# Optimization experiments

Hardware: AMD Instinct MI355X
Metric: run time of the kernel (lower is better)

## Reference

```python
import jax, jax.numpy as jnp
import numpy as np

D_MODEL = 2048
N_HEADS = 16
N_KV_HEADS = 4
D_K = D_MODEL // N_HEADS  # 128
N_REP = N_HEADS // N_KV_HEADS  # 4
EPS = 1e-8
ROPE_BASE = 10000.0


def setup_inputs() -> dict:
    key = jax.random.key(0)
    ks = jax.random.split(key, 6)
    B, S = 2, 2048
    s_in = 1.0 / np.sqrt(D_MODEL)
    return {
        "x": jax.random.normal(ks[0], (B, S, D_MODEL), jnp.float32),
        "Wq": jax.random.normal(ks[1], (D_MODEL, D_MODEL), jnp.float32) * s_in,
        "bq": jnp.zeros((D_MODEL,), jnp.float32),
        "Wk": jax.random.normal(ks[2], (N_KV_HEADS * D_K, D_MODEL), jnp.float32) * s_in,
        "bk": jnp.zeros((N_KV_HEADS * D_K,), jnp.float32),
        "Wv": jax.random.normal(ks[3], (N_KV_HEADS * D_K, D_MODEL), jnp.float32) * s_in,
        "bv": jnp.zeros((N_KV_HEADS * D_K,), jnp.float32),
        "Wo": jax.random.normal(ks[4], (D_MODEL, D_MODEL), jnp.float32) * s_in,
        "bo": jnp.zeros((D_MODEL,), jnp.float32),
        "q_norm_w": jnp.ones((D_K,), jnp.float32),
        "k_norm_w": jnp.ones((D_K,), jnp.float32),
    }


def _rmsnorm(x, w):
    rms = jnp.sqrt(jnp.mean(x * x, axis=-1, keepdims=True) + EPS)
    return x / rms * w


def _rope(x, cos, sin):
    # x: [B, S, H, d_k]; interleaved pair rotation (pairs along last dim)
    B, S, H, d = x.shape
    xr = x.reshape(B, S, H, d // 2, 2)
    x1, x2 = xr[..., 0], xr[..., 1]
    c = cos[:, None, :]  # [S, 1, d/2] -> broadcasts over [B, S, H, d/2]
    s = sin[:, None, :]
    o1 = x1 * c - x2 * s
    o2 = x1 * s + x2 * c
    return jnp.stack([o1, o2], axis=-1).reshape(B, S, H, d)


def reference(x, Wq, bq, Wk, bk, Wv, bv, Wo, bo, q_norm_w, k_norm_w):
    B, S, D = x.shape
    scale = 1.0 / np.sqrt(D_K)

    q = (x @ Wq.T + bq).reshape(B, S, N_HEADS, D_K)
    k = (x @ Wk.T + bk).reshape(B, S, N_KV_HEADS, D_K)
    v = (x @ Wv.T + bv).reshape(B, S, N_KV_HEADS, D_K)

    q = _rmsnorm(q, q_norm_w)
    k = _rmsnorm(k, k_norm_w)

    # RoPE tables (cos/sin of t * inv_freq), shape [S, d_k/2]
    inv_freq = 1.0 / (ROPE_BASE ** (jnp.arange(0, D_K, 2, dtype=jnp.float32) / D_K))
    freqs = jnp.arange(S, dtype=jnp.float32)[:, None] * inv_freq[None, :]
    cos, sin = jnp.cos(freqs), jnp.sin(freqs)
    q = _rope(q, cos, sin)
    k = _rope(k, cos, sin)

    # [B, H, S, d]
    q = q.transpose(0, 2, 1, 3)
    k = k.transpose(0, 2, 1, 3)
    v = v.transpose(0, 2, 1, 3)

    # GQA: group q heads by kv head instead of repeating k/v
    qg = q.reshape(B, N_KV_HEADS, N_REP, S, D_K)
    scores = jnp.einsum("bkrqd,bkld->bkrql", qg, k) * scale
    causal = jnp.tril(jnp.ones((S, S), dtype=bool))  # [S, S]
    scores = jnp.where(causal, scores, jnp.float32(-1e9))
    attn = jax.nn.softmax(scores, axis=-1)
    out = jnp.einsum("bkrql,bkld->bkrqd", attn, v)  # [B, Hk, rep, S, d]
    out = out.reshape(B, N_HEADS, S, D_K).transpose(0, 2, 1, 3).reshape(B, S, D)
    return out @ Wo.T + bo
```

## Files before the change

### kernel.cpp

```cpp
#include <hip/hip_runtime.h>
#include <hip/hip_bf16.h>
#include <stdint.h>

#define DM 2048
#define SQ 2048
#define NB 2
#define NH 16
#define NKV 4
#define DK 128
#define NQKV 3072

typedef unsigned short u16;
typedef unsigned int u32;
typedef __attribute__((ext_vector_type(8))) __bf16 bf16x8;
typedef __attribute__((ext_vector_type(4))) float f32x4;
typedef __attribute__((ext_vector_type(8))) u16 u16x8;
typedef __attribute__((ext_vector_type(2))) u32 u32x2;

__device__ __forceinline__ u16 f2bf(float f) {
  u32 x = __builtin_bit_cast(u32, f);
  x += 0x7fffu + ((x >> 16) & 1u);
  return (u16)(x >> 16);
}

__device__ __forceinline__ float bf2f(u16 h) {
  u32 x = ((u32)h) << 16;
  return __builtin_bit_cast(float, x);
}

__device__ __forceinline__ f32x4 mfma16(bf16x8 a, bf16x8 b, f32x4 c) {
  return __builtin_amdgcn_mfma_f32_16x16x32_bf16(a, b, c, 0, 0, 0);
}

#define GLDS16(g, l)                                                          \
  __builtin_amdgcn_global_load_lds(                                           \
      (const __attribute__((address_space(1))) void*)(g),                     \
      (__attribute__((address_space(3))) void*)(l), 16, 0, 0)

#define N_CAST 2359296
#define N_ROPE (SQ * 64)
__global__ void setup_all(const float* __restrict__ x, const float* __restrict__ Wq,
                          const float* __restrict__ Wk, const float* __restrict__ Wv,
                          const float* __restrict__ Wo, const float* __restrict__ bq,
                          const float* __restrict__ bk, const float* __restrict__ bv,
                          u16* __restrict__ xb, u16* __restrict__ Wqkvb, u16* __restrict__ Wob,
                          float* __restrict__ ct, float* __restrict__ st_,
                          float* __restrict__ fb) {
  int i = blockIdx.x * blockDim.x + threadIdx.x;
  if (i < N_CAST) {
    const float* src;
    u16* dst;
    int j;
    if (i < 1048576) { src = x; dst = xb; j = i; }
    else if (i < 1572864) { src = Wq; dst = Wqkvb; j = i - 1048576; }
    else if (i < 1703936) { src = Wk; dst = Wqkvb + (size_t)DM * DM; j = i - 1572864; }
    else if (i < 1835008) { src = Wv; dst = Wqkvb + (size_t)(DM + NKV * DK) * DM; j = i - 1703936; }
    else { src = Wo; dst = Wob; j = i - 1835008; }
    const float4* s4 = (const float4*)src;
    float4 a = s4[2 * j], b = s4[2 * j + 1];
    u16x8 v;
    v[0] = f2bf(a.x); v[1] = f2bf(a.y); v[2] = f2bf(a.z); v[3] = f2bf(a.w);
    v[4] = f2bf(b.x); v[5] = f2bf(b.y); v[6] = f2bf(b.z); v[7] = f2bf(b.w);
    *(u16x8*)(dst + 8 * (size_t)j) = v;
  } else if (i < N_CAST + N_ROPE) {
    int j = i - N_CAST;
    int s = j >> 6, d = j & 63;
    float theta = (float)s * __expf((float)d * (-9.2103403720f / 64.0f));
    float sn, cs;
    sincosf(theta, &sn, &cs);
    ct[j] = cs;
    st_[j] = sn;
  } else if (i < N_CAST + N_ROPE + NQKV) {
    int j = i - N_CAST - N_ROPE;
    float v;
    if (j < DM) v = bq[j];
    else if (j < DM + NKV * DK) v = bk[j - DM];
    else v = bv[j - DM - NKV * DK];
    fb[j] = v;
  }
}

__global__ __launch_bounds__(256) void gemm_bt(
    const u16* __restrict__ A, const u16* __restrict__ W,
    const float* __restrict__ bias, void* __restrict__ Cv,
    int M, int N, int K, int obf16) {
  __shared__ u16 As[128 * 64];
  __shared__ u16 Bs[128 * 64];
  const int tid = threadIdx.x;
  const int w = tid >> 6, l = tid & 63;
  const int hi = l >> 4, lo = l & 15;
  const int MB = M >> 7;
  const int bm = blockIdx.x % MB, bn = blockIdx.x / MB;
  const int wr = w >> 1, wc = w & 1;
  const int lr8 = l >> 3, lc = l & 7;
  f32x4 acc[4][4] = {};
  for (int kt = 0; kt < K; kt += 64) {
#pragma unroll
    for (int i = 0; i < 4; ++i) {
      int row = w * 32 + i * 8 + lr8;
      int gc = lc ^ (row & 7);
      GLDS16(A + (size_t)(bm * 128 + row) * K + kt + gc * 8, &As[(w * 32 + i * 8) * 64]);
    }
#pragma unroll
    for (int i = 0; i < 4; ++i) {
      int row = w * 32 + i * 8 + lr8;
      int gc = lc ^ (row & 7);
      GLDS16(W + (size_t)(bn * 128 + row) * K + kt + gc * 8, &Bs[(w * 32 + i * 8) * 64]);
    }
    __syncthreads();
#pragma unroll
    for (int kk = 0; kk < 2; ++kk) {
      bf16x8 af[4], bf[4];
#pragma unroll
      for (int mi = 0; mi < 4; ++mi) {
        int row = wr * 64 + mi * 16 + lo;
        af[mi] = *(const bf16x8*)&As[row * 64 + (((kk * 4 + hi) ^ (row & 7)) * 8)];
      }
#pragma unroll
      for (int ni = 0; ni < 4; ++ni) {
        int row = wc * 64 + ni * 16 + lo;
        bf[ni] = *(const bf16x8*)&Bs[row * 64 + (((kk * 4 + hi) ^ (row & 7)) * 8)];
      }
#pragma unroll
      for (int mi = 0; mi < 4; ++mi)
#pragma unroll
        for (int ni = 0; ni < 4; ++ni)
          acc[mi][ni] = mfma16(af[mi], bf[ni], acc[mi][ni]);
    }
    __syncthreads();
  }
#pragma unroll
  for (int mi = 0; mi < 4; ++mi) {
#pragma unroll
    for (int ni = 0; ni < 4; ++ni) {
      int col = bn * 128 + wc * 64 + ni * 16 + lo;
      float bv = bias[col];
#pragma unroll
      for (int r = 0; r < 4; ++r) {
        int rowg = bm * 128 + wr * 64 + mi * 16 + hi * 4 + r;
        float val = acc[mi][ni][r] + bv;
        if (obf16)
          ((u16*)Cv)[(size_t)rowg * N + col] = f2bf(val);
        else
          ((float*)Cv)[(size_t)rowg * N + col] = val;
      }
    }
  }
}

__global__ void normrope_qk(const u16* __restrict__ qkv,
                            const float* __restrict__ qw, const float* __restrict__ kw,
                            const float* __restrict__ cosT, const float* __restrict__ sinT,
                            u16* __restrict__ qb, u16* __restrict__ kb) {
  int gw = (int)((blockIdx.x * (size_t)blockDim.x + threadIdx.x) >> 6);
  int lane = threadIdx.x & 63;
  int bs = gw / (NH + NKV), j = gw % (NH + NKV);
  int b = bs / SQ, s = bs % SQ;
  const u16* src;
  const float* wgt;
  u16* dst;
  float post = 1.0f;
  if (j < NH) {
    src = qkv + (size_t)bs * NQKV + j * DK;
    wgt = qw;
    dst = qb + ((size_t)(b * NH + j) * SQ + s) * DK;
    post = 0.08838834764831845f;
  } else {
    int kh = j - NH;
    src = qkv + (size_t)bs * NQKV + DM + kh * DK;
    wgt = kw;
    dst = kb + ((size_t)(b * NKV + kh) * SQ + s) * DK;
  }
  u32 pk = *(const u32*)(src + 2 * lane);
  float xv0 = bf2f((u16)(pk & 0xffff));
  float xv1 = bf2f((u16)(pk >> 16));
  float ss = xv0 * xv0 + xv1 * xv1;
#pragma unroll
  for (int m = 1; m < 64; m <<= 1) ss += __shfl_xor(ss, m);
  float inv = rsqrtf(ss * (1.0f / DK) + 1e-8f);
  float x1 = xv0 * inv * wgt[2 * lane];
  float x2 = xv1 * inv * wgt[2 * lane + 1];
  float cs = cosT[s * 64 + lane];
  float sn = sinT[s * 64 + lane];
  float o1 = (x1 * cs - x2 * sn) * post;
  float o2 = (x1 * sn + x2 * cs) * post;
  u32 pack = (u32)f2bf(o1) | ((u32)f2bf(o2) << 16);
  *(u32*)(dst + 2 * lane) = pack;
}

__global__ __launch_bounds__(256) void vtrans(const u16* __restrict__ qkv, u16* __restrict__ vt) {
  __shared__ u16 T[128 * 72];
  int bid = blockIdx.x;
  int st = bid % (SQ / 64);
  int rem = bid / (SQ / 64);
  int vh = rem % NKV, b = rem / NKV;
  int s0 = st * 64;
  int t = threadIdx.x;
#pragma unroll
  for (int it = 0; it < 4; ++it) {
    int idx = it * 256 + t;
    int sl = idx >> 4;
    int c = idx & 15;
    u16x8 v = *(const u16x8*)(qkv + (size_t)(b * SQ + s0 + sl) * NQKV + DM + NKV * DK + vh * DK + c * 8);
#pragma unroll
    for (int e = 0; e < 8; ++e) T[(c * 8 + e) * 72 + sl] = v[e];
  }
  __syncthreads();
#pragma unroll
  for (int it = 0; it < 4; ++it) {
    int idx = it * 256 + t;
    int d = idx >> 3;
    int ch = idx & 7;
    u16x8 v = *(const u16x8*)&T[d * 72 + ch * 8];
    *(u16x8*)(vt + ((size_t)(b * NKV + vh) * DK + d) * SQ + s0 + ch * 8) = v;
  }
}

__global__ __launch_bounds__(256) void attn(const u16* __restrict__ qb, const u16* __restrict__ kb,
                                            const u16* __restrict__ vt, u16* __restrict__ out) {
  __shared__ u16 Ks[2][64 * 128];
  __shared__ u16 Vs[2][128 * 64];
  __shared__ u16 P[4][16 * 64];
  const int w = threadIdx.x >> 6, l = threadIdx.x & 63;
  const int hi = l >> 4, lo = l & 15;
  const int pr = blockIdx.x, h = blockIdx.y, b = blockIdx.z;
  const int kvh = h >> 2;
  const u16* Q = qb + (size_t)(b * NH + h) * SQ * DK;
  const u16* K = kb + (size_t)(b * NKV + kvh) * SQ * DK;
  const u16* V = vt + (size_t)(b * NKV + kvh) * DK * SQ;

  auto stageKV = [&](int buf, int kt) {
#pragma unroll
    for (int i = 0; i < 4; ++i) {
      int rb = w * 16 + i * 4;
      int row = rb + (l >> 4);
      int gc = (l & 15) ^ (row & 7);
      GLDS16(K + (size_t)(kt + row) * DK + gc * 8, &Ks[buf][rb * 128]);
    }
#pragma unroll
    for (int i = 0; i < 4; ++i) {
      int rb = w * 32 + i * 8;
      int row = rb + (l >> 3);
      int gc = (l & 7) ^ (row & 7);
      GLDS16(V + (size_t)row * SQ + kt + gc * 8, &Vs[buf][rb * 64]);
    }
  };

#pragma unroll 1
  for (int seg = 0; seg < 2; ++seg) {
    const int qt = seg ? (SQ / 64 - 1 - pr) : pr;
    const int q0 = qt * 64 + w * 16;
    bf16x8 qf[4];
#pragma unroll
    for (int kk = 0; kk < 4; ++kk)
      qf[kk] = *(const bf16x8*)(Q + (size_t)(q0 + lo) * DK + kk * 32 + hi * 8);
    f32x4 oacc[8] = {};
    float lrun = 0.f;
    const int nt = qt + 1;
    stageKV(0, 0);
    __syncthreads();
#pragma unroll 1
    for (int ti = 0; ti < nt; ++ti) {
      const int cur = ti & 1;
      if (ti + 1 < nt) stageKV(cur ^ 1, (ti + 1) * 64);
      const int kt = ti * 64;
      f32x4 sfr[4];
      __builtin_amdgcn_s_setprio(1);
#pragma unroll
      for (int cb = 0; cb < 4; ++cb) {
        f32x4 sf = {};
#pragma unroll
        for (int kk = 0; kk < 4; ++kk) {
          int row = cb * 16 + lo;
          bf16x8 kfr = *(const bf16x8*)&Ks[cur][row * 128 + (((kk * 4 + hi) ^ (row & 7)) * 8)];
          sf = mfma16(kfr, qf[kk], sf);
        }
        sfr[cb] = sf;
      }
      __builtin_amdgcn_s_setprio(0);
      if (ti == nt - 1) {
#pragma unroll
        for (int cb = 0; cb < 4; ++cb)
#pragma unroll
          for (int r = 0; r < 4; ++r) {
            int kcol = kt + cb * 16 + hi * 4 + r;
            if (kcol > q0 + lo) sfr[cb][r] = -1e9f;
          }
      }
      float rs = 0.f;
#pragma unroll
      for (int cb = 0; cb < 4; ++cb) {
        float p0 = __expf(sfr[cb][0] - 12.0f);
        float p1 = __expf(sfr[cb][1] - 12.0f);
        float p2 = __expf(sfr[cb][2] - 12.0f);
        float p3 = __expf(sfr[cb][3] - 12.0f);
        rs += (p0 + p1) + (p2 + p3);
        u32x2 pw;
        pw[0] = (u32)f2bf(p0) | ((u32)f2bf(p1) << 16);
        pw[1] = (u32)f2bf(p2) | ((u32)f2bf(p3) << 16);
        int chunk = cb * 2 + (hi >> 1);
        *(u32x2*)&P[w][lo * 64 + ((chunk ^ (lo & 7)) * 8) + (hi & 1) * 4] = pw;
      }
      rs += __shfl_xor(rs, 16);
      rs += __shfl_xor(rs, 32);
      lrun += rs;
      __builtin_amdgcn_s_setprio(1);
#pragma unroll
      for (int half = 0; half < 2; ++half) {
        bf16x8 pa = *(const bf16x8*)&P[w][lo * 64 + (((half * 4 + hi) ^ (lo & 7)) * 8)];
#pragma unroll
        for (int fr = 0; fr < 8; ++fr) {
          int row = fr * 16 + lo;
          bf16x8 vfr = *(const bf16x8*)&Vs[cur][row * 64 + (((half * 4 + hi) ^ (row & 7)) * 8)];
          oacc[fr] = mfma16(pa, vfr, oacc[fr]);
        }
      }
      __builtin_amdgcn_s_setprio(0);
      __syncthreads();
    }
    float invl = 1.0f / lrun;
    float invlB[4];
#pragma unroll
    for (int r = 0; r < 4; ++r) invlB[r] = __shfl(invl, hi * 4 + r);
#pragma unroll
    for (int fr = 0; fr < 8; ++fr) {
#pragma unroll
      for (int r = 0; r < 4; ++r) {
        int row = b * SQ + q0 + hi * 4 + r;
        int col = h * DK + fr * 16 + lo;
        out[(size_t)row * DM + col] = f2bf(oacc[fr][r] * invlB[r]);
      }
    }
  }
}

extern "C" void kernel_launch(void* const* d_in, const int* in_sizes, int n_in,
                              void* d_out, int out_size, void* d_ws, size_t ws_size,
                              hipStream_t stream) {
  const float* x = (const float*)d_in[0];
  const float* Wq = (const float*)d_in[1];
  const float* bq = (const float*)d_in[2];
  const float* Wk = (const float*)d_in[3];
  const float* bk = (const float*)d_in[4];
  const float* Wv = (const float*)d_in[5];
  const float* bv = (const float*)d_in[6];
  const float* Wo = (const float*)d_in[7];
  const float* bo = (const float*)d_in[8];
  const float* qw = (const float*)d_in[9];
  const float* kw = (const float*)d_in[10];
  float* outp = (float*)d_out;

  char* ws = (char*)d_ws;
  size_t off = 0;
  auto alloc = [&](size_t bytes) {
    char* p = ws + off;
    off += (bytes + 255) & ~(size_t)255;
    return p;
  };
  u16* xb = (u16*)alloc((size_t)NB * SQ * DM * 2);
  u16* Wqkvb = (u16*)alloc((size_t)NQKV * DM * 2);
  u16* Wob = (u16*)alloc((size_t)DM * DM * 2);
  float* fbias = (float*)alloc((size_t)NQKV * 4);
  float* cosT = (float*)alloc((size_t)SQ * 64 * 4);
  float* sinT = (float*)alloc((size_t)SQ * 64 * 4);
  u16* qkvb = (u16*)alloc((size_t)NB * SQ * NQKV * 2);
  u16* qbh = (u16*)alloc((size_t)NB * NH * SQ * DK * 2);
  u16* kbh = (u16*)alloc((size_t)NB * NKV * SQ * DK * 2);
  u16* vth = (u16*)alloc((size_t)NB * NKV * DK * SQ * 2);
  u16* aout = (u16*)alloc((size_t)NB * SQ * DM * 2);

  {
    int total = N_CAST + N_ROPE + NQKV;
    setup_all<<<(total + 255) / 256, 256, 0, stream>>>(x, Wq, Wk, Wv, Wo, bq, bk, bv,
                                                       xb, Wqkvb, Wob, cosT, sinT, fbias);
  }
  {
    int M = NB * SQ;
    gemm_bt<<<(M / 128) * (NQKV / 128), 256, 0, stream>>>(xb, Wqkvb, fbias, qkvb, M, NQKV, DM, 1);
  }
  {
    int waves = NB * SQ * (NH + NKV);
    normrope_qk<<<waves / 4, 256, 0, stream>>>(qkvb, qw, kw, cosT, sinT, qbh, kbh);
    vtrans<<<NB * NKV * (SQ / 64), 256, 0, stream>>>(qkvb, vth);
  }
  {
    dim3 g(SQ / 128, NH, NB);
    attn<<<g, 256, 0, stream>>>(qbh, kbh, vth, aout);
  }
  {
    int M = NB * SQ;
    gemm_bt<<<(M / 128) * (DM / 128), 256, 0, stream>>>(aout, Wob, bo, outp, M, DM, DM, 0);
  }
}
```

Measured before the change: 216.8 us.

## Split attention waves 2x2 over query and key halves with LDS reduction

Each attention block's four waves now form a 2x2 grid. Every wave handles 32 query rows (two 16-row groups) against one 32-column half of each 64-key tile, so each K and V fragment read from LDS feeds two MFMAs. Waves whose key half lies entirely above the causal diagonal skip their compute. The two key-half partial outputs and row sums are combined through LDS at the end. This doubles accumulator registers and adds an LDS reduction and an extra barrier per segment, in exchange for less LDS traffic per MFMA and some causal work skipping.

```diff
diff --git a/kernel.cpp b/kernel.cpp
--- a/kernel.cpp
+++ b/kernel.cpp
@@ -220,9 +220,10 @@
                                             const u16* __restrict__ vt, u16* __restrict__ out) {
   __shared__ u16 Ks[2][64 * 128];
   __shared__ u16 Vs[2][128 * 64];
-  __shared__ u16 P[4][16 * 64];
+  __shared__ u16 P[8][16 * 32];
   const int w = threadIdx.x >> 6, l = threadIdx.x & 63;
   const int hi = l >> 4, lo = l & 15;
+  const int wq = w >> 1, wk = w & 1;
   const int pr = blockIdx.x, h = blockIdx.y, b = blockIdx.z;
   const int kvh = h >> 2;
   const u16* Q = qb + (size_t)(b * NH + h) * SQ * DK;
@@ -249,14 +250,17 @@
 #pragma unroll 1
   for (int seg = 0; seg < 2; ++seg) {
     const int qt = seg ? (SQ / 64 - 1 - pr) : pr;
-    const int q0 = qt * 64 + w * 16;
-    bf16x8 qf[4];
-#pragma unroll
-    for (int kk = 0; kk < 4; ++kk)
-      qf[kk] = *(const bf16x8*)(Q + (size_t)(q0 + lo) * DK + kk * 32 + hi * 8);
-    f32x4 oacc[8] = {};
-    float lrun = 0.f;
+    const int qbase = qt * 64 + wq * 32;
+    bf16x8 qf[2][4];
+#pragma unroll
+    for (int g = 0; g < 2; ++g)
+#pragma unroll
+      for (int kk = 0; kk < 4; ++kk)
+        qf[g][kk] = *(const bf16x8*)(Q + (size_t)(qbase + g * 16 + lo) * DK + kk * 32 + hi * 8);
+    f32x4 oacc[2][8] = {};
+    float lrun[2] = {0.f, 0.f};
     const int nt = qt + 1;
+    __syncthreads();
     stageKV(0, 0);
     __syncthreads();
 #pragma unroll 1
@@ -264,71 +268,107 @@
       const int cur = ti & 1;
       if (ti + 1 < nt) stageKV(cur ^ 1, (ti + 1) * 64);
       const int kt = ti * 64;
-      f32x4 sfr[4];
-      __builtin_amdgcn_s_setprio(1);
-#pragma unroll
-      for (int cb = 0; cb < 4; ++cb) {
-        f32x4 sf = {};
-#pragma unroll
-        for (int kk = 0; kk < 4; ++kk) {
-          int row = cb * 16 + lo;
-          bf16x8 kfr = *(const bf16x8*)&Ks[cur][row * 128 + (((kk * 4 + hi) ^ (row & 7)) * 8)];
-          sf = mfma16(kfr, qf[kk], sf);
+      const int ktw = kt + wk * 32;
+      if (ktw <= qbase + 31) {
+        f32x4 sfr[2][2];
+        __builtin_amdgcn_s_setprio(1);
+#pragma unroll
+        for (int cbl = 0; cbl < 2; ++cbl) {
+          f32x4 sf0 = {}, sf1 = {};
+#pragma unroll
+          for (int kk = 0; kk < 4; ++kk) {
+            int row = wk * 32 + cbl * 16 + lo;
+            bf16x8 kfr = *(const bf16x8*)&Ks[cur][row * 128 + (((kk * 4 + hi) ^ (row & 7)) * 8)];
+            sf0 = mfma16(kfr, qf[0][kk], sf0);
+            sf1 = mfma16(kfr, qf[1][kk], sf1);
+          }
+          sfr[0][cbl] = sf0;
+          sfr[1][cbl] = sf1;
         }
-        sfr[cb] = sf;
-      }
-      __builtin_amdgcn_s_setprio(0);
-      if (ti == nt - 1) {
-#pragma unroll
-        for (int cb = 0; cb < 4; ++cb)
-#pragma unroll
-          for (int r = 0; r < 4; ++r) {
-            int kcol = kt + cb * 16 + hi * 4 + r;
-            if (kcol > q0 + lo) sfr[cb][r] = -1e9f;
+        __builtin_amdgcn_s_setprio(0);
+#pragma unroll
+        for (int g = 0; g < 2; ++g) {
+          int q0 = qbase + g * 16;
+          if (ktw + 31 > q0) {
+#pragma unroll
+            for (int cbl = 0; cbl < 2; ++cbl)
+#pragma unroll
+              for (int r = 0; r < 4; ++r) {
+                int kcol = ktw + cbl * 16 + hi * 4 + r;
+                if (kcol > q0 + lo) sfr[g][cbl][r] = -1e9f;
+              }
           }
-      }
-      float rs = 0.f;
-#pragma unroll
-      for (int cb = 0; cb < 4; ++cb) {
-        float p0 = __expf(sfr[cb][0] - 12.0f);
-        float p1 = __expf(sfr[cb][1] - 12.0f);
-        float p2 = __expf(sfr[cb][2] - 12.0f);
-        float p3 = __expf(sfr[cb][3] - 12.0f);
-        rs += (p0 + p1) + (p2 + p3);
-        u32x2 pw;
-        pw[0] = (u32)f2bf(p0) | ((u32)f2bf(p1) << 16);
-        pw[1] = (u32)f2bf(p2) | ((u32)f2bf(p3) << 16);
-        int chunk = cb * 2 + (hi >> 1);
-        *(u32x2*)&P[w][lo * 64 + ((chunk ^ (lo & 7)) * 8) + (hi & 1) * 4] = pw;
-      }
-      rs += __shfl_xor(rs, 16);
-      rs += __shfl_xor(rs, 32);
-      lrun += rs;
-      __builtin_amdgcn_s_setprio(1);
-#pragma unroll
-      for (int half = 0; half < 2; ++half) {
-        bf16x8 pa = *(const bf16x8*)&P[w][lo * 64 + (((half * 4 + hi) ^ (lo & 7)) * 8)];
+        }
+#pragma unroll
+        for (int g = 0; g < 2; ++g) {
+          float rs = 0.f;
+#pragma unroll
+          for (int cbl = 0; cbl < 2; ++cbl) {
+            float p0 = __expf(sfr[g][cbl][0] - 12.0f);
+            float p1 = __expf(sfr[g][cbl][1] - 12.0f);
+            float p2 = __expf(sfr[g][cbl][2] - 12.0f);
+            float p3 = __expf(sfr[g][cbl][3] - 12.0f);
+            rs += (p0 + p1) + (p2 + p3);
+            u32x2 pw;
+            pw[0] = (u32)f2bf(p0) | ((u32)f2bf(p1) << 16);
+            pw[1] = (u32)f2bf(p2) | ((u32)f2bf(p3) << 16);
+            int chunk = cbl * 2 + (hi >> 1);
+            *(u32x2*)&P[w * 2 + g][lo * 32 + ((chunk ^ (lo & 3)) * 8) + (hi & 1) * 4] = pw;
+          }
+          rs += __shfl_xor(rs, 16);
+          rs += __shfl_xor(rs, 32);
+          lrun[g] += rs;
+        }
+        __builtin_amdgcn_s_setprio(1);
+        bf16x8 pa0 = *(const bf16x8*)&P[w * 2 + 0][lo * 32 + ((hi ^ (lo & 3)) * 8)];
+        bf16x8 pa1 = *(const bf16x8*)&P[w * 2 + 1][lo * 32 + ((hi ^ (lo & 3)) * 8)];
 #pragma unroll
         for (int fr = 0; fr < 8; ++fr) {
           int row = fr * 16 + lo;
-          bf16x8 vfr = *(const bf16x8*)&Vs[cur][row * 64 + (((half * 4 + hi) ^ (row & 7)) * 8)];
-          oacc[fr] = mfma16(pa, vfr, oacc[fr]);
+          bf16x8 vfr = *(const bf16x8*)&Vs[cur][row * 64 + (((wk * 4 + hi) ^ (row & 7)) * 8)];
+          oacc[0][fr] = mfma16(pa0, vfr, oacc[0][fr]);
+          oacc[1][fr] = mfma16(pa1, vfr, oacc[1][fr]);
         }
+        __builtin_amdgcn_s_setprio(0);
       }
-      __builtin_amdgcn_s_setprio(0);
       __syncthreads();
     }
-    float invl = 1.0f / lrun;
-    float invlB[4];
-#pragma unroll
-    for (int r = 0; r < 4; ++r) invlB[r] = __shfl(invl, hi * 4 + r);
-#pragma unroll
-    for (int fr = 0; fr < 8; ++fr) {
-#pragma unroll
-      for (int r = 0; r < 4; ++r) {
-        int row = b * SQ + q0 + hi * 4 + r;
-        int col = h * DK + fr * 16 + lo;
-        out[(size_t)row * DM + col] = f2bf(oacc[fr][r] * invlB[r]);
+    float* sc = (float*)Ks;
+    float* sc2 = (float*)Vs;
+    if (wk == 1) {
+      int base = wq * 4096 + l * 64;
+#pragma unroll
+      for (int g = 0; g < 2; ++g)
+#pragma unroll
+        for (int fr = 0; fr < 8; ++fr)
+          *(f32x4*)&sc[base + (g * 8 + fr) * 4] = oacc[g][fr];
+      sc2[wq * 128 + l] = lrun[0];
+      sc2[wq * 128 + 64 + l] = lrun[1];
+    }
+    __syncthreads();
+    if (wk == 0) {
+      int base = wq * 4096 + l * 64;
+#pragma unroll
+      for (int g = 0; g < 2; ++g)
+#pragma unroll
+        for (int fr = 0; fr < 8; ++fr)
+          oacc[g][fr] += *(const f32x4*)&sc[base + (g * 8 + fr) * 4];
+#pragma unroll
+      for (int g = 0; g < 2; ++g) {
+        float lsum = lrun[g] + sc2[wq * 128 + g * 64 + l];
+        float invl = 1.0f / lsum;
+        float invlB[4];
+#pragma unroll
+        for (int r = 0; r < 4; ++r) invlB[r] = __shfl(invl, hi * 4 + r);
+#pragma unroll
+        for (int fr = 0; fr < 8; ++fr) {
+#pragma unroll
+          for (int r = 0; r < 4; ++r) {
+            int row = b * SQ + qbase + g * 16 + hi * 4 + r;
+            int col = h * DK + fr * 16 + lo;
+            out[(size_t)row * DM + col] = f2bf(oacc[g][fr][r] * invlB[r]);
+          }
+        }
       }
     }
   }
```

Result: slower. 229.1 us (+5.7%).

## Restructure attention: one q-tile per block, register P shuffle, split K/V staging

Applied to the files above, without the earlier changes.

The attention kernel now assigns one 64-row query tile per block (32 blocks along x, heaviest tiles first) instead of pairing a short and a long tile per block. The P matrix moves from registers to MFMA operand layout with cross-lane shuffles instead of a round trip through shared memory. V is single-buffered and loaded separately from double-buffered K, with explicit vmcnt waits and raw barriers. This cuts LDS traffic and footprint, which could raise occupancy, but doubles the block count and gives up the pairing's load balance.

```diff
diff --git a/kernel.cpp b/kernel.cpp
--- a/kernel.cpp
+++ b/kernel.cpp
@@ -15,7 +15,7 @@
 typedef __attribute__((ext_vector_type(8))) __bf16 bf16x8;
 typedef __attribute__((ext_vector_type(4))) float f32x4;
 typedef __attribute__((ext_vector_type(8))) u16 u16x8;
-typedef __attribute__((ext_vector_type(2))) u32 u32x2;
+typedef __attribute__((ext_vector_type(4))) u32 u32x4;
 
 __device__ __forceinline__ u16 f2bf(float f) {
   u32 x = __builtin_bit_cast(u32, f);
@@ -219,17 +219,16 @@
 __global__ __launch_bounds__(256) void attn(const u16* __restrict__ qb, const u16* __restrict__ kb,
                                             const u16* __restrict__ vt, u16* __restrict__ out) {
   __shared__ u16 Ks[2][64 * 128];
-  __shared__ u16 Vs[2][128 * 64];
-  __shared__ u16 P[4][16 * 64];
+  __shared__ u16 Vs[128 * 64];
   const int w = threadIdx.x >> 6, l = threadIdx.x & 63;
   const int hi = l >> 4, lo = l & 15;
-  const int pr = blockIdx.x, h = blockIdx.y, b = blockIdx.z;
+  const int qt = 31 - (int)blockIdx.x, h = blockIdx.y, b = blockIdx.z;
   const int kvh = h >> 2;
   const u16* Q = qb + (size_t)(b * NH + h) * SQ * DK;
   const u16* K = kb + (size_t)(b * NKV + kvh) * SQ * DK;
   const u16* V = vt + (size_t)(b * NKV + kvh) * DK * SQ;
 
-  auto stageKV = [&](int buf, int kt) {
+  auto stageK = [&](int buf, int kt) {
 #pragma unroll
     for (int i = 0; i < 4; ++i) {
       int rb = w * 16 + i * 4;
@@ -237,99 +236,125 @@
       int gc = (l & 15) ^ (row & 7);
       GLDS16(K + (size_t)(kt + row) * DK + gc * 8, &Ks[buf][rb * 128]);
     }
+  };
+  auto stageV = [&](int kt) {
 #pragma unroll
     for (int i = 0; i < 4; ++i) {
       int rb = w * 32 + i * 8;
       int row = rb + (l >> 3);
       int gc = (l & 7) ^ (row & 7);
-      GLDS16(V + (size_t)row * SQ + kt + gc * 8, &Vs[buf][rb * 64]);
+      GLDS16(V + (size_t)row * SQ + kt + gc * 8, &Vs[rb * 64]);
     }
   };
 
+  const int q0 = qt * 64 + w * 16;
+  bf16x8 qf[4];
+#pragma unroll
+  for (int kk = 0; kk < 4; ++kk)
+    qf[kk] = *(const bf16x8*)(Q + (size_t)(q0 + lo) * DK + kk * 32 + hi * 8);
+  f32x4 oacc[8] = {};
+  float lrun = 0.f;
+  const int nt = qt + 1;
+
+  stageK(0, 0);
+  asm volatile("s_waitcnt vmcnt(0)" ::: "memory");
+  __builtin_amdgcn_sched_barrier(0);
+  __builtin_amdgcn_s_barrier();
+  __builtin_amdgcn_sched_barrier(0);
+
 #pragma unroll 1
-  for (int seg = 0; seg < 2; ++seg) {
-    const int qt = seg ? (SQ / 64 - 1 - pr) : pr;
-    const int q0 = qt * 64 + w * 16;
-    bf16x8 qf[4];
-#pragma unroll
-    for (int kk = 0; kk < 4; ++kk)
-      qf[kk] = *(const bf16x8*)(Q + (size_t)(q0 + lo) * DK + kk * 32 + hi * 8);
-    f32x4 oacc[8] = {};
-    float lrun = 0.f;
-    const int nt = qt + 1;
-    stageKV(0, 0);
-    __syncthreads();
-#pragma unroll 1
-    for (int ti = 0; ti < nt; ++ti) {
-      const int cur = ti & 1;
-      if (ti + 1 < nt) stageKV(cur ^ 1, (ti + 1) * 64);
-      const int kt = ti * 64;
-      f32x4 sfr[4];
-      __builtin_amdgcn_s_setprio(1);
-#pragma unroll
-      for (int cb = 0; cb < 4; ++cb) {
-        f32x4 sf = {};
-#pragma unroll
-        for (int kk = 0; kk < 4; ++kk) {
-          int row = cb * 16 + lo;
-          bf16x8 kfr = *(const bf16x8*)&Ks[cur][row * 128 + (((kk * 4 + hi) ^ (row & 7)) * 8)];
-          sf = mfma16(kfr, qf[kk], sf);
+  for (int ti = 0; ti < nt; ++ti) {
+    const int cur = ti & 1;
+    const int kt = ti * 64;
+    const bool pk = (ti + 1 < nt);
+    stageV(kt);
+    if (pk) stageK(cur ^ 1, kt + 64);
+    if (pk) asm volatile("s_waitcnt vmcnt(8)" ::: "memory");
+    else    asm volatile("s_waitcnt vmcnt(4)" ::: "memory");
+    __builtin_amdgcn_sched_barrier(0);
+    __builtin_amdgcn_s_barrier();
+    __builtin_amdgcn_sched_barrier(0);
+    f32x4 sfr[4];
+    __builtin_amdgcn_s_setprio(1);
+#pragma unroll
+    for (int cb = 0; cb < 4; ++cb) {
+      f32x4 sf = {};
+#pragma unroll
+      for (int kk = 0; kk < 4; ++kk) {
+        int row = cb * 16 + lo;
+        bf16x8 kfr = *(const bf16x8*)&Ks[cur][row * 128 + (((kk * 4 + hi) ^ (row & 7)) * 8)];
+        sf = mfma16(kfr, qf[kk], sf);
+      }
+      sfr[cb] = sf;
+    }
+    __builtin_amdgcn_s_setprio(0);
+    if (ti == nt - 1) {
+#pragma unroll
+      for (int cb = 0; cb < 4; ++cb)
+#pragma unroll
+        for (int r = 0; r < 4; ++r) {
+          int kcol = kt + cb * 16 + hi * 4 + r;
+          if (kcol > q0 + lo) sfr[cb][r] = -1e9f;
         }
-        sfr[cb] = sf;
+    }
+    u32 pu[4][2];
+    float rs = 0.f;
+#pragma unroll
+    for (int cb = 0; cb < 4; ++cb) {
+      float p0 = __expf(sfr[cb][0] - 12.0f);
+      float p1 = __expf(sfr[cb][1] - 12.0f);
+      float p2 = __expf(sfr[cb][2] - 12.0f);
+      float p3 = __expf(sfr[cb][3] - 12.0f);
+      rs += (p0 + p1) + (p2 + p3);
+      pu[cb][0] = (u32)f2bf(p0) | ((u32)f2bf(p1) << 16);
+      pu[cb][1] = (u32)f2bf(p2) | ((u32)f2bf(p3) << 16);
+    }
+    rs += __shfl_xor(rs, 16);
+    rs += __shfl_xor(rs, 32);
+    lrun += rs;
+    if (pk) asm volatile("s_waitcnt vmcnt(4)" ::: "memory");
+    else    asm volatile("s_waitcnt vmcnt(0)" ::: "memory");
+    __builtin_amdgcn_sched_barrier(0);
+    __builtin_amdgcn_s_barrier();
+    __builtin_amdgcn_sched_barrier(0);
+    __builtin_amdgcn_s_setprio(1);
+    const int srcA = ((2 * hi) & 3) * 16 + lo;
+    const int srcB = ((2 * hi + 1) & 3) * 16 + lo;
+    const bool sel = (hi & 2) != 0;
+#pragma unroll
+    for (int h2 = 0; h2 < 2; ++h2) {
+      u32 a0l = __shfl(pu[h2 * 2][0], srcA), a0h = __shfl(pu[h2 * 2 + 1][0], srcA);
+      u32 a1l = __shfl(pu[h2 * 2][1], srcA), a1h = __shfl(pu[h2 * 2 + 1][1], srcA);
+      u32 b0l = __shfl(pu[h2 * 2][0], srcB), b0h = __shfl(pu[h2 * 2 + 1][0], srcB);
+      u32 b1l = __shfl(pu[h2 * 2][1], srcB), b1h = __shfl(pu[h2 * 2 + 1][1], srcB);
+      u32x4 paw;
+      paw[0] = sel ? a0h : a0l;
+      paw[1] = sel ? a1h : a1l;
+      paw[2] = sel ? b0h : b0l;
+      paw[3] = sel ? b1h : b1l;
+      bf16x8 pa = __builtin_bit_cast(bf16x8, paw);
+#pragma unroll
+      for (int fr = 0; fr < 8; ++fr) {
+        int row = fr * 16 + lo;
+        bf16x8 vfr = *(const bf16x8*)&Vs[row * 64 + (((h2 * 4 + hi) ^ (row & 7)) * 8)];
+        oacc[fr] = mfma16(pa, vfr, oacc[fr]);
       }
-      __builtin_amdgcn_s_setprio(0);
-      if (ti == nt - 1) {
-#pragma unroll
-        for (int cb = 0; cb < 4; ++cb)
-#pragma unroll
-          for (int r = 0; r < 4; ++r) {
-            int kcol = kt + cb * 16 + hi * 4 + r;
-            if (kcol > q0 + lo) sfr[cb][r] = -1e9f;
-          }
-      }
-      float rs = 0.f;
-#pragma unroll
-      for (int cb = 0; cb < 4; ++cb) {
-        float p0 = __expf(sfr[cb][0] - 12.0f);
-        float p1 = __expf(sfr[cb][1] - 12.0f);
-        float p2 = __expf(sfr[cb][2] - 12.0f);
-        float p3 = __expf(sfr[cb][3] - 12.0f);
-        rs += (p0 + p1) + (p2 + p3);
-        u32x2 pw;
-        pw[0] = (u32)f2bf(p0) | ((u32)f2bf(p1) << 16);
-        pw[1] = (u32)f2bf(p2) | ((u32)f2bf(p3) << 16);
-        int chunk = cb * 2 + (hi >> 1);
-        *(u32x2*)&P[w][lo * 64 + ((chunk ^ (lo & 7)) * 8) + (hi & 1) * 4] = pw;
-      }
-      rs += __shfl_xor(rs, 16);
-      rs += __shfl_xor(rs, 32);
-      lrun += rs;
-      __builtin_amdgcn_s_setprio(1);
-#pragma unroll
-      for (int half = 0; half < 2; ++half) {
-        bf16x8 pa = *(const bf16x8*)&P[w][lo * 64 + (((half * 4 + hi) ^ (lo & 7)) * 8)];
-#pragma unroll
-        for (int fr = 0; fr < 8; ++fr) {
-          int row = fr * 16 + lo;
-          bf16x8 vfr = *(const bf16x8*)&Vs[cur][row * 64 + (((half * 4 + hi) ^ (row & 7)) * 8)];
-          oacc[fr] = mfma16(pa, vfr, oacc[fr]);
-        }
-      }
-      __builtin_amdgcn_s_setprio(0);
-      __syncthreads();
-    }
-    float invl = 1.0f / lrun;
-    float invlB[4];
-#pragma unroll
-    for (int r = 0; r < 4; ++r) invlB[r] = __shfl(invl, hi * 4 + r);
-#pragma unroll
-    for (int fr = 0; fr < 8; ++fr) {
-#pragma unroll
-      for (int r = 0; r < 4; ++r) {
-        int row = b * SQ + q0 + hi * 4 + r;
-        int col = h * DK + fr * 16 + lo;
-        out[(size_t)row * DM + col] = f2bf(oacc[fr][r] * invlB[r]);
-      }
+    }
+    __builtin_amdgcn_s_setprio(0);
+    __builtin_amdgcn_s_barrier();
+    __builtin_amdgcn_sched_barrier(0);
+  }
+  float invl = 1.0f / lrun;
+  float invlB[4];
+#pragma unroll
+  for (int r = 0; r < 4; ++r) invlB[r] = __shfl(invl, hi * 4 + r);
+#pragma unroll
+  for (int fr = 0; fr < 8; ++fr) {
+#pragma unroll
+    for (int r = 0; r < 4; ++r) {
+      int row = b * SQ + q0 + hi * 4 + r;
+      int col = h * DK + fr * 16 + lo;
+      out[(size_t)row * DM + col] = f2bf(oacc[fr][r] * invlB[r]);
     }
   }
 }
@@ -384,7 +409,7 @@
     vtrans<<<NB * NKV * (SQ / 64), 256, 0, stream>>>(qkvb, vth);
   }
   {
-    dim3 g(SQ / 128, NH, NB);
+    dim3 g(32, NH, NB);
     attn<<<g, 256, 0, stream>>>(qbh, kbh, vth, aout);
   }
   {
```

Result: slower. 272.5 us (+25.7%).

## Fuse QK RMSNorm and RoPE into the QKV GEMM epilogue

Applied to the files above, without the earlier changes.

The QKV projection GEMM epilogue now applies RMSNorm, RoPE and the query scale for Q and K column tiles, writing head-major bf16 Q/K directly. Each 128-column tile is exactly one head, so the row sum of squares is reduced with lane shuffles plus a shared-memory exchange between the two column waves. The separate normrope kernel launch and its read of the Q/K part of the qkv buffer go away. In exchange the epilogue gets heavier, with more shuffles, scattered 2-byte stores and cos/sin gathers that may be uncoalesced.

```diff
diff --git a/kernel.cpp b/kernel.cpp
--- a/kernel.cpp
+++ b/kernel.cpp
@@ -83,7 +83,10 @@
 __global__ __launch_bounds__(256) void gemm_bt(
     const u16* __restrict__ A, const u16* __restrict__ W,
     const float* __restrict__ bias, void* __restrict__ Cv,
-    int M, int N, int K, int obf16) {
+    int M, int N, int K, int mode,
+    const float* __restrict__ qw, const float* __restrict__ kw,
+    const float* __restrict__ cosT, const float* __restrict__ sinT,
+    u16* __restrict__ qdst, u16* __restrict__ kdst) {
   __shared__ u16 As[128 * 64];
   __shared__ u16 Bs[128 * 64];
   const int tid = threadIdx.x;
@@ -130,62 +133,106 @@
     __syncthreads();
   }
 #pragma unroll
+  for (int ni = 0; ni < 4; ++ni) {
+    float bvv = bias[bn * 128 + wc * 64 + ni * 16 + lo];
+#pragma unroll
+    for (int mi = 0; mi < 4; ++mi)
+#pragma unroll
+      for (int r = 0; r < 4; ++r) acc[mi][ni][r] += bvv;
+  }
+  if (mode == 0) {
+#pragma unroll
+    for (int mi = 0; mi < 4; ++mi)
+#pragma unroll
+      for (int ni = 0; ni < 4; ++ni) {
+        int col = bn * 128 + wc * 64 + ni * 16 + lo;
+#pragma unroll
+        for (int r = 0; r < 4; ++r) {
+          int rowg = bm * 128 + wr * 64 + mi * 16 + hi * 4 + r;
+          ((float*)Cv)[(size_t)rowg * N + col] = acc[mi][ni][r];
+        }
+      }
+    return;
+  }
+  if (bn >= 20) {
+#pragma unroll
+    for (int mi = 0; mi < 4; ++mi)
+#pragma unroll
+      for (int ni = 0; ni < 4; ++ni) {
+        int col = bn * 128 + wc * 64 + ni * 16 + lo;
+#pragma unroll
+        for (int r = 0; r < 4; ++r) {
+          int rowg = bm * 128 + wr * 64 + mi * 16 + hi * 4 + r;
+          ((u16*)Cv)[(size_t)rowg * N + col] = f2bf(acc[mi][ni][r]);
+        }
+      }
+    return;
+  }
+  f32x4 pr4[4];
+#pragma unroll
   for (int mi = 0; mi < 4; ++mi) {
-#pragma unroll
-    for (int ni = 0; ni < 4; ++ni) {
-      int col = bn * 128 + wc * 64 + ni * 16 + lo;
-      float bv = bias[col];
-#pragma unroll
-      for (int r = 0; r < 4; ++r) {
-        int rowg = bm * 128 + wr * 64 + mi * 16 + hi * 4 + r;
-        float val = acc[mi][ni][r] + bv;
-        if (obf16)
-          ((u16*)Cv)[(size_t)rowg * N + col] = f2bf(val);
-        else
-          ((float*)Cv)[(size_t)rowg * N + col] = val;
-      }
-    }
-  }
-}
-
-__global__ void normrope_qk(const u16* __restrict__ qkv,
-                            const float* __restrict__ qw, const float* __restrict__ kw,
-                            const float* __restrict__ cosT, const float* __restrict__ sinT,
-                            u16* __restrict__ qb, u16* __restrict__ kb) {
-  int gw = (int)((blockIdx.x * (size_t)blockDim.x + threadIdx.x) >> 6);
-  int lane = threadIdx.x & 63;
-  int bs = gw / (NH + NKV), j = gw % (NH + NKV);
-  int b = bs / SQ, s = bs % SQ;
-  const u16* src;
-  const float* wgt;
-  u16* dst;
-  float post = 1.0f;
-  if (j < NH) {
-    src = qkv + (size_t)bs * NQKV + j * DK;
-    wgt = qw;
-    dst = qb + ((size_t)(b * NH + j) * SQ + s) * DK;
-    post = 0.08838834764831845f;
-  } else {
-    int kh = j - NH;
-    src = qkv + (size_t)bs * NQKV + DM + kh * DK;
-    wgt = kw;
-    dst = kb + ((size_t)(b * NKV + kh) * SQ + s) * DK;
-  }
-  u32 pk = *(const u32*)(src + 2 * lane);
-  float xv0 = bf2f((u16)(pk & 0xffff));
-  float xv1 = bf2f((u16)(pk >> 16));
-  float ss = xv0 * xv0 + xv1 * xv1;
-#pragma unroll
-  for (int m = 1; m < 64; m <<= 1) ss += __shfl_xor(ss, m);
-  float inv = rsqrtf(ss * (1.0f / DK) + 1e-8f);
-  float x1 = xv0 * inv * wgt[2 * lane];
-  float x2 = xv1 * inv * wgt[2 * lane + 1];
-  float cs = cosT[s * 64 + lane];
-  float sn = sinT[s * 64 + lane];
-  float o1 = (x1 * cs - x2 * sn) * post;
-  float o2 = (x1 * sn + x2 * cs) * post;
-  u32 pack = (u32)f2bf(o1) | ((u32)f2bf(o2) << 16);
-  *(u32*)(dst + 2 * lane) = pack;
+    f32x4 p = acc[mi][0] * acc[mi][0];
+    p += acc[mi][1] * acc[mi][1];
+    p += acc[mi][2] * acc[mi][2];
+    p += acc[mi][3] * acc[mi][3];
+    pr4[mi] = p;
+  }
+#pragma unroll
+  for (int mask = 1; mask < 16; mask <<= 1)
+#pragma unroll
+    for (int mi = 0; mi < 4; ++mi)
+#pragma unroll
+      for (int c = 0; c < 4; ++c) pr4[mi][c] += __shfl_xor(pr4[mi][c], mask);
+  float* Sred = (float*)As;
+  if (lo == 0) {
+#pragma unroll
+    for (int mi = 0; mi < 4; ++mi)
+#pragma unroll
+      for (int r = 0; r < 4; ++r)
+        Sred[wc * 128 + wr * 64 + mi * 16 + hi * 4 + r] = pr4[mi][r];
+  }
+  __syncthreads();
+  float inv_[4][4];
+#pragma unroll
+  for (int mi = 0; mi < 4; ++mi)
+#pragma unroll
+    for (int r = 0; r < 4; ++r) {
+      int row = wr * 64 + mi * 16 + hi * 4 + r;
+      float ss = Sred[row] + Sred[128 + row];
+      inv_[mi][r] = rsqrtf(ss * (1.0f / DK) + 1e-8f);
+    }
+  const bool isq = (bn < 16);
+  const float* wgt = isq ? qw : kw;
+  float wgtv[4];
+#pragma unroll
+  for (int ni = 0; ni < 4; ++ni) wgtv[ni] = wgt[wc * 64 + ni * 16 + lo];
+  const float post = isq ? 0.08838834764831845f : 1.0f;
+  const int b = (bm * 128) >> 11;
+  const size_t hb = isq ? ((size_t)(b * NH + bn) * SQ) : ((size_t)(b * NKV + (bn - 16)) * SQ);
+  u16* dstp = isq ? qdst : kdst;
+  const bool odd = (lo & 1);
+#pragma unroll
+  for (int mi = 0; mi < 4; ++mi) {
+#pragma unroll
+    for (int r = 0; r < 4; ++r) {
+      int row = wr * 64 + mi * 16 + hi * 4 + r;
+      int srow = (bm * 128 + row) & (SQ - 1);
+      float iv = inv_[mi][r];
+#pragma unroll
+      for (int ni = 0; ni < 4; ++ni) {
+        int colh = wc * 64 + ni * 16 + lo;
+        float vn = acc[mi][ni][r] * iv * wgtv[ni];
+        float pn = __shfl_xor(vn, 1);
+        float x1 = odd ? pn : vn;
+        float x2 = odd ? vn : pn;
+        int d2 = colh >> 1;
+        float cs = cosT[srow * 64 + d2];
+        float sn = sinT[srow * 64 + d2];
+        float o = odd ? (x1 * sn + x2 * cs) : (x1 * cs - x2 * sn);
+        dstp[(hb + srow) * DK + colh] = f2bf(o * post);
+      }
+    }
+  }
 }
 
 __global__ __launch_bounds__(256) void vtrans(const u16* __restrict__ qkv, u16* __restrict__ vt) {
@@ -376,19 +423,17 @@
   }
   {
     int M = NB * SQ;
-    gemm_bt<<<(M / 128) * (NQKV / 128), 256, 0, stream>>>(xb, Wqkvb, fbias, qkvb, M, NQKV, DM, 1);
-  }
-  {
-    int waves = NB * SQ * (NH + NKV);
-    normrope_qk<<<waves / 4, 256, 0, stream>>>(qkvb, qw, kw, cosT, sinT, qbh, kbh);
-    vtrans<<<NB * NKV * (SQ / 64), 256, 0, stream>>>(qkvb, vth);
-  }
+    gemm_bt<<<(M / 128) * (NQKV / 128), 256, 0, stream>>>(
+        xb, Wqkvb, fbias, qkvb, M, NQKV, DM, 1, qw, kw, cosT, sinT, qbh, kbh);
+  }
+  vtrans<<<NB * NKV * (SQ / 64), 256, 0, stream>>>(qkvb, vth);
   {
     dim3 g(SQ / 128, NH, NB);
     attn<<<g, 256, 0, stream>>>(qbh, kbh, vth, aout);
   }
   {
     int M = NB * SQ;
-    gemm_bt<<<(M / 128) * (DM / 128), 256, 0, stream>>>(aout, Wob, bo, outp, M, DM, DM, 0);
-  }
-}
+    gemm_bt<<<(M / 128) * (DM / 128), 256, 0, stream>>>(
+        aout, Wob, bo, outp, M, DM, DM, 0, nullptr, nullptr, nullptr, nullptr, nullptr, nullptr);
+  }
+}
```

Measured after the change: 219.8 us. About the same (+1.4%).
